# Kernel tuning notes

Measured on AMD Instinct MI355X. Metric: run time of the kernel, lower is better.

## Reference

```python
import jax, jax.numpy as jnp
import numpy as np

H = 512  # hidden_dim

def setup_inputs() -> dict:
    key = jax.random.key(0)
    k1, k2, k3, k4, k5 = jax.random.split(key, 5)
    B, S = 32, 2048
    hidden = jax.random.normal(k1, (B, 2 * H), dtype=jnp.float32)
    encoder_outputs = jax.random.normal(k2, (B, S, 2 * H), dtype=jnp.float32)
    # nn.Linear(4H, H): weight [H, 4H], bias [H]
    W = jax.random.normal(k3, (H, 4 * H), dtype=jnp.float32) / np.sqrt(4 * H)
    b = jnp.zeros((H,), dtype=jnp.float32)
    v = jax.random.normal(k4, (H,), dtype=jnp.float32) / np.sqrt(H)
    return {"hidden": hidden, "encoder_outputs": encoder_outputs, "W": W, "b": b, "v": v}

def reference(hidden, encoder_outputs, W, b, v):
    B, S, _ = encoder_outputs.shape
    # concat repeated decoder hidden with encoder outputs: [B, S, 4H]
    hidden_rep = jnp.broadcast_to(hidden[:, None, :], (B, S, hidden.shape[-1]))
    cat = jnp.concatenate([hidden_rep, encoder_outputs], axis=-1)
    energy = jnp.tanh(jnp.einsum('bsf,hf->bsh', cat, W) + b)  # [B, S, H]
    scores = jnp.einsum('bsh,h->bs', energy, v)               # [B, S]
    attn = jax.nn.softmax(scores, axis=1)                     # softmax over seq
    context = jnp.einsum('bsd,bs->bd', encoder_outputs, attn) # [B, 2H]
    return context
```

## Files before the change

### kernel.cpp

```cpp
#include <hip/hip_runtime.h>


typedef __fp16   half2v __attribute__((ext_vector_type(2)));
typedef _Float16 half8  __attribute__((ext_vector_type(8)));
typedef __attribute__((ext_vector_type(4)))  float f4;
typedef __attribute__((ext_vector_type(16))) float f16v;
typedef __attribute__((ext_vector_type(4)))  unsigned int uint4v;

__device__ __forceinline__ void gload_lds16(const void* g, void* l) {
    __builtin_amdgcn_global_load_lds(
        (const __attribute__((address_space(1))) unsigned int*)g,
        (__attribute__((address_space(3))) unsigned int*)l, 16, 0, 0);
}
__device__ __forceinline__ unsigned int bc2(half2v h) {
    return __builtin_bit_cast(unsigned int, h);
}

__global__ __launch_bounds__(256) void prep_kernel(
    const float* __restrict__ hidden, const float* __restrict__ W,
    const float* __restrict__ bias, float* __restrict__ u,
    unsigned short* __restrict__ w2) {
    if (blockIdx.x < 64) {
        int t = blockIdx.x * 256 + threadIdx.x;
        int b = t >> 9, h = t & 511;
        const f4* wr = (const f4*)(W + (size_t)h * 2048);
        const f4* hr = (const f4*)(hidden + (size_t)b * 1024);
        float acc = bias[h];
        #pragma unroll 4
        for (int i = 0; i < 256; ++i) {
            f4 w4 = wr[i]; f4 h4 = hr[i];
            acc += w4[0]*h4[0] + w4[1]*h4[1] + w4[2]*h4[2] + w4[3]*h4[3];
        }
        u[t] = acc;
    } else {
        int g = (blockIdx.x - 64) * 256 + threadIdx.x;
        int kk = g >> 11, id = g & 2047;
        int ntg = id >> 7, kh = (id >> 6) & 1, l = id & 63;
        int h = (ntg << 5) + (l & 31);
        int kg = 1024 + (kk << 5) + (kh << 4) + ((l >> 5) << 3);
        const float* src = W + (size_t)h * 2048 + kg;
        f4 x0 = *(const f4*)src;
        f4 x1 = *(const f4*)(src + 4);
        half8 vh;
        #pragma unroll
        for (int j = 0; j < 4; ++j) vh[j] = (_Float16)x0[j];
        #pragma unroll
        for (int j = 0; j < 4; ++j) vh[4 + j] = (_Float16)x1[j];
        ((half8*)w2)[g] = vh;
    }
}

__global__ __launch_bounds__(256, 3) void score_kernel(
    const float* __restrict__ enc, const unsigned short* __restrict__ w2,
    const float* __restrict__ u, const float* __restrict__ v,
    float* __restrict__ scores_part) {
    __shared__ short Ahi[2048], Alo[2048];
    __shared__ short Bs[8192];
    __shared__ float u_s[256], v_s[256];
    __shared__ float partial[4][64];

    const int tid  = threadIdx.x;
    const int wl   = tid >> 6, lane = tid & 63;
    const int col  = lane & 31;
    const int sblk = blockIdx.x >> 1, hh = blockIdx.x & 1;
    const int row0 = sblk * 64;
    const int b    = row0 >> 11;
    const float* encB = enc + (size_t)row0 * 1024;

    u_s[tid] = u[(b << 9) + (hh << 8) + tid];
    v_s[tid] = v[(hh << 8) + tid];

    f16v acc[2][2];
    #pragma unroll
    for (int mt = 0; mt < 2; ++mt)
        #pragma unroll
        for (int nt = 0; nt < 2; ++nt)
            #pragma unroll
            for (int r = 0; r < 16; ++r) acc[mt][nt][r] = 0.f;

    const int s_mt = tid >> 7, s_kh = (tid >> 6) & 1, s_l = tid & 63;
    const int s_row = (s_mt << 5) + (s_l & 31);
    const int s_kb  = (s_kh << 4) + ((s_l >> 5) << 3);
    const float* aSrc = encB + (size_t)s_row * 1024 + s_kb;

    const half8* Ah8 = (const half8*)Ahi;
    const half8* Al8 = (const half8*)Alo;
    const half8* Bh8 = (const half8*)Bs;

    for (int kk = 0; kk < 32; ++kk) {
        f4 x0 = *(const f4*)(aSrc + (kk << 5));
        f4 x1 = *(const f4*)(aSrc + (kk << 5) + 4);
        __syncthreads();
        {
            half2v h01 = __builtin_amdgcn_cvt_pkrtz(x0[0], x0[1]);
            half2v h23 = __builtin_amdgcn_cvt_pkrtz(x0[2], x0[3]);
            half2v h45 = __builtin_amdgcn_cvt_pkrtz(x1[0], x1[1]);
            half2v h67 = __builtin_amdgcn_cvt_pkrtz(x1[2], x1[3]);
            half2v l01 = __builtin_amdgcn_cvt_pkrtz(x0[0] - (float)h01[0], x0[1] - (float)h01[1]);
            half2v l23 = __builtin_amdgcn_cvt_pkrtz(x0[2] - (float)h23[0], x0[3] - (float)h23[1]);
            half2v l45 = __builtin_amdgcn_cvt_pkrtz(x1[0] - (float)h45[0], x1[1] - (float)h45[1]);
            half2v l67 = __builtin_amdgcn_cvt_pkrtz(x1[2] - (float)h67[0], x1[3] - (float)h67[1]);
            uint4v hp = {bc2(h01), bc2(h23), bc2(h45), bc2(h67)};
            uint4v lp = {bc2(l01), bc2(l23), bc2(l45), bc2(l67)};
            ((uint4v*)Ahi)[tid] = hp;
            ((uint4v*)Alo)[tid] = lp;
        }
        {
            const char* bsrc = (const char*)w2 + (size_t)kk * 32768 + (hh << 14)
                               + (wl << 12) + lane * 16;
            char* bdst = (char*)Bs + (wl << 12);
            #pragma unroll
            for (int i = 0; i < 4; ++i)
                gload_lds16(bsrc + (i << 10), bdst + (i << 10));
        }
        __syncthreads();
        #pragma unroll
        for (int kh = 0; kh < 2; ++kh) {
            half8 ah0 = Ah8[(kh << 6) + lane];
            half8 ah1 = Ah8[128 + (kh << 6) + lane];
            half8 al0 = Al8[(kh << 6) + lane];
            half8 al1 = Al8[128 + (kh << 6) + lane];
            #pragma unroll
            for (int nt = 0; nt < 2; ++nt) {
                int ntl = (wl << 1) + nt;
                half8 b8 = Bh8[((ntl << 1) + kh) * 64 + lane];
                acc[0][nt] = __builtin_amdgcn_mfma_f32_32x32x16_f16(ah0, b8, acc[0][nt], 0, 0, 0);
                acc[0][nt] = __builtin_amdgcn_mfma_f32_32x32x16_f16(al0, b8, acc[0][nt], 0, 0, 0);
                acc[1][nt] = __builtin_amdgcn_mfma_f32_32x32x16_f16(ah1, b8, acc[1][nt], 0, 0, 0);
                acc[1][nt] = __builtin_amdgcn_mfma_f32_32x32x16_f16(al1, b8, acc[1][nt], 0, 0, 0);
            }
        }
    }
    const int rhalf = (lane >> 5) << 2;
    #pragma unroll
    for (int mt = 0; mt < 2; ++mt) {
        #pragma unroll
        for (int reg = 0; reg < 16; ++reg) {
            float ssum = 0.f;
            #pragma unroll
            for (int nt = 0; nt < 2; ++nt) {
                int hl = (((wl << 1) + nt) << 5) + col;
                float x = u_s[hl] + acc[mt][nt][reg];
                float t = __expf(2.f * x);
                float th = 1.f - 2.f / (t + 1.f);
                ssum += v_s[hl] * th;
            }
            ssum += __shfl_xor(ssum, 1);
            ssum += __shfl_xor(ssum, 2);
            ssum += __shfl_xor(ssum, 4);
            ssum += __shfl_xor(ssum, 8);
            ssum += __shfl_xor(ssum, 16);
            if (col == 0)
                partial[wl][(mt << 5) + (reg & 3) + ((reg >> 2) << 3) + rhalf] = ssum;
        }
    }
    __syncthreads();
    if (tid < 64) {
        float s = partial[0][tid] + partial[1][tid] + partial[2][tid] + partial[3][tid];
        scores_part[(hh << 16) + row0 + tid] = s;
    }
}

__global__ __launch_bounds__(256) void ctx_partial_kernel(
    const float* __restrict__ enc, const float* __restrict__ scores_part,
    float* __restrict__ partials) {
    __shared__ float p_s[2048];
    __shared__ float wredm[4], wreds[4];
    const int t = threadIdx.x;
    const int b = blockIdx.x >> 5, sc = blockIdx.x & 31;
    const int wid = t >> 6, lane = t & 63;
    const float* s0 = scores_part + ((size_t)b << 11);
    const float* s1 = s0 + 65536;

    float vals[8];
    float mx = -1e30f;
    #pragma unroll
    for (int i = 0; i < 8; ++i) {
        int idx = t + (i << 8);
        vals[i] = s0[idx] + s1[idx];
        mx = fmaxf(mx, vals[i]);
    }
    #pragma unroll
    for (int off = 1; off < 64; off <<= 1) mx = fmaxf(mx, __shfl_xor(mx, off));
    if (lane == 0) wredm[wid] = mx;
    __syncthreads();
    mx = fmaxf(fmaxf(wredm[0], wredm[1]), fmaxf(wredm[2], wredm[3]));

    float lsum = 0.f;
    #pragma unroll
    for (int i = 0; i < 8; ++i) {
        float e = __expf(vals[i] - mx);
        p_s[t + (i << 8)] = e;
        lsum += e;
    }
    #pragma unroll
    for (int off = 1; off < 64; off <<= 1) lsum += __shfl_xor(lsum, off);
    if (lane == 0) wreds[wid] = lsum;
    __syncthreads();
    const float inv = 1.f / (wreds[0] + wreds[1] + wreds[2] + wreds[3]);

    f4 a = (f4){0.f, 0.f, 0.f, 0.f};
    const f4* erow = ((const f4*)(enc + ((size_t)b * 2048 + (sc << 6)) * 1024)) + t;
    #pragma unroll 4
    for (int i = 0; i < 64; ++i) {
        float p = p_s[(sc << 6) + i] * inv;
        f4 e = erow[(size_t)i << 8];
        a += p * e;
    }
    f4* dst = (f4*)(partials + (((size_t)(sc << 5) + b) << 10));
    dst[t] = a;
}

__global__ __launch_bounds__(256) void ctx_reduce_kernel(
    const float* __restrict__ partials, float* __restrict__ out) {
    int i = blockIdx.x * 256 + threadIdx.x;
    float s = 0.f;
    #pragma unroll
    for (int sc = 0; sc < 32; ++sc) s += partials[sc * 32768 + i];
    out[i] = s;
}

extern "C" void kernel_launch(void* const* d_in, const int* in_sizes, int n_in,
                              void* d_out, int out_size, void* d_ws, size_t ws_size,
                              hipStream_t stream) {
    const float* hidden = (const float*)d_in[0];
    const float* enc    = (const float*)d_in[1];
    const float* W      = (const float*)d_in[2];
    const float* bias   = (const float*)d_in[3];
    const float* v      = (const float*)d_in[4];
    float* out = (float*)d_out;
    char* ws = (char*)d_ws;

    float* u            = (float*)(ws);
    float* scores_part  = (float*)(ws + 65536);
    float* partials     = (float*)(ws + 589824);
    unsigned short* w2  = (unsigned short*)(ws + 4784128);

    prep_kernel<<<320, 256, 0, stream>>>(hidden, W, bias, u, w2);
    score_kernel<<<2048, 256, 0, stream>>>(enc, w2, u, v, scores_part);
    ctx_partial_kernel<<<1024, 256, 0, stream>>>(enc, scores_part, partials);
    ctx_reduce_kernel<<<128, 256, 0, stream>>>(partials, out);
}
```

Measured before the change: 548.0 us.

## Double-buffer score GEMM LDS, warp-parallel u projection, dual accumulators in context

The score kernel's K loop becomes software-pipelined. A and B tiles are double-buffered in LDS, the B tile for the next step is prefetched with global-to-LDS loads, and A registers are prefetched two steps ahead. Manual waitcnt plus a single barrier per step replaces the two __syncthreads, and MFMA priority is raised. The prep kernel's hidden·W projection now uses one wavefront per output row with coalesced loads and shuffle reduction instead of one thread per output. The context partial loop gets two accumulators, with the normalisation moved out of the loop. Doubled LDS use may lower occupancy of the 3-blocks-per-CU score kernel.

```diff
diff --git a/kernel.cpp b/kernel.cpp
--- a/kernel.cpp
+++ b/kernel.cpp
@@ -15,25 +15,15 @@
 __device__ __forceinline__ unsigned int bc2(half2v h) {
     return __builtin_bit_cast(unsigned int, h);
 }
+#define MEMPIN asm volatile("" ::: "memory")
 
 __global__ __launch_bounds__(256) void prep_kernel(
     const float* __restrict__ hidden, const float* __restrict__ W,
     const float* __restrict__ bias, float* __restrict__ u,
     unsigned short* __restrict__ w2) {
-    if (blockIdx.x < 64) {
-        int t = blockIdx.x * 256 + threadIdx.x;
-        int b = t >> 9, h = t & 511;
-        const f4* wr = (const f4*)(W + (size_t)h * 2048);
-        const f4* hr = (const f4*)(hidden + (size_t)b * 1024);
-        float acc = bias[h];
-        #pragma unroll 4
-        for (int i = 0; i < 256; ++i) {
-            f4 w4 = wr[i]; f4 h4 = hr[i];
-            acc += w4[0]*h4[0] + w4[1]*h4[1] + w4[2]*h4[2] + w4[3]*h4[3];
-        }
-        u[t] = acc;
-    } else {
-        int g = (blockIdx.x - 64) * 256 + threadIdx.x;
+    __shared__ float hid_s[1024];
+    if (blockIdx.x < 256) {
+        int g = blockIdx.x * 256 + threadIdx.x;
         int kk = g >> 11, id = g & 2047;
         int ntg = id >> 7, kh = (id >> 6) & 1, l = id & 63;
         int h = (ntg << 5) + (l & 31);
@@ -47,6 +37,29 @@
         #pragma unroll
         for (int j = 0; j < 4; ++j) vh[4 + j] = (_Float16)x1[j];
         ((half8*)w2)[g] = vh;
+    } else {
+        const int t = threadIdx.x;
+        const int blk = (int)blockIdx.x - 256;
+        const int b = blk >> 3, hg = blk & 7;
+        ((f4*)hid_s)[t] = ((const f4*)(hidden + ((size_t)b << 10)))[t];
+        __syncthreads();
+        const int w = t >> 6, lane = t & 63;
+        const f4* hid4 = (const f4*)hid_s;
+        #pragma unroll 2
+        for (int i = 0; i < 16; ++i) {
+            int h = (hg << 6) + (w << 4) + i;
+            const f4* wr = (const f4*)(W + (size_t)h * 2048);
+            float p = 0.f;
+            #pragma unroll
+            for (int i2 = 0; i2 < 4; ++i2) {
+                f4 w4 = wr[lane + (i2 << 6)];
+                f4 h4 = hid4[lane + (i2 << 6)];
+                p += w4[0]*h4[0] + w4[1]*h4[1] + w4[2]*h4[2] + w4[3]*h4[3];
+            }
+            #pragma unroll
+            for (int off = 1; off < 64; off <<= 1) p += __shfl_xor(p, off);
+            if (lane == 0) u[((size_t)b << 9) + h] = bias[h] + p;
+        }
     }
 }
 
@@ -54,8 +67,8 @@
     const float* __restrict__ enc, const unsigned short* __restrict__ w2,
     const float* __restrict__ u, const float* __restrict__ v,
     float* __restrict__ scores_part) {
-    __shared__ short Ahi[2048], Alo[2048];
-    __shared__ short Bs[8192];
+    __shared__ short Ahi[2][2048], Alo[2][2048];
+    __shared__ short Bs[2][8192];
     __shared__ float u_s[256], v_s[256];
     __shared__ float partial[4][64];
 
@@ -83,54 +96,99 @@
     const int s_kb  = (s_kh << 4) + ((s_l >> 5) << 3);
     const float* aSrc = encB + (size_t)s_row * 1024 + s_kb;
 
-    const half8* Ah8 = (const half8*)Ahi;
-    const half8* Al8 = (const half8*)Alo;
-    const half8* Bh8 = (const half8*)Bs;
-
-    for (int kk = 0; kk < 32; ++kk) {
-        f4 x0 = *(const f4*)(aSrc + (kk << 5));
-        f4 x1 = *(const f4*)(aSrc + (kk << 5) + 4);
-        __syncthreads();
-        {
-            half2v h01 = __builtin_amdgcn_cvt_pkrtz(x0[0], x0[1]);
-            half2v h23 = __builtin_amdgcn_cvt_pkrtz(x0[2], x0[3]);
-            half2v h45 = __builtin_amdgcn_cvt_pkrtz(x1[0], x1[1]);
-            half2v h67 = __builtin_amdgcn_cvt_pkrtz(x1[2], x1[3]);
-            half2v l01 = __builtin_amdgcn_cvt_pkrtz(x0[0] - (float)h01[0], x0[1] - (float)h01[1]);
-            half2v l23 = __builtin_amdgcn_cvt_pkrtz(x0[2] - (float)h23[0], x0[3] - (float)h23[1]);
-            half2v l45 = __builtin_amdgcn_cvt_pkrtz(x1[0] - (float)h45[0], x1[1] - (float)h45[1]);
-            half2v l67 = __builtin_amdgcn_cvt_pkrtz(x1[2] - (float)h67[0], x1[3] - (float)h67[1]);
-            uint4v hp = {bc2(h01), bc2(h23), bc2(h45), bc2(h67)};
-            uint4v lp = {bc2(l01), bc2(l23), bc2(l45), bc2(l67)};
-            ((uint4v*)Ahi)[tid] = hp;
-            ((uint4v*)Alo)[tid] = lp;
-        }
-        {
-            const char* bsrc = (const char*)w2 + (size_t)kk * 32768 + (hh << 14)
-                               + (wl << 12) + lane * 16;
-            char* bdst = (char*)Bs + (wl << 12);
-            #pragma unroll
-            for (int i = 0; i < 4; ++i)
-                gload_lds16(bsrc + (i << 10), bdst + (i << 10));
-        }
-        __syncthreads();
-        #pragma unroll
-        for (int kh = 0; kh < 2; ++kh) {
-            half8 ah0 = Ah8[(kh << 6) + lane];
-            half8 ah1 = Ah8[128 + (kh << 6) + lane];
-            half8 al0 = Al8[(kh << 6) + lane];
-            half8 al1 = Al8[128 + (kh << 6) + lane];
-            #pragma unroll
-            for (int nt = 0; nt < 2; ++nt) {
-                int ntl = (wl << 1) + nt;
-                half8 b8 = Bh8[((ntl << 1) + kh) * 64 + lane];
-                acc[0][nt] = __builtin_amdgcn_mfma_f32_32x32x16_f16(ah0, b8, acc[0][nt], 0, 0, 0);
-                acc[0][nt] = __builtin_amdgcn_mfma_f32_32x32x16_f16(al0, b8, acc[0][nt], 0, 0, 0);
-                acc[1][nt] = __builtin_amdgcn_mfma_f32_32x32x16_f16(ah1, b8, acc[1][nt], 0, 0, 0);
-                acc[1][nt] = __builtin_amdgcn_mfma_f32_32x32x16_f16(al1, b8, acc[1][nt], 0, 0, 0);
-            }
-        }
-    }
+#define STAGE_B(buf, kkex) do {                                               \
+        const char* bsrc_ = (const char*)w2 + (size_t)(kkex) * 32768          \
+                            + (hh << 14) + (wl << 12) + lane * 16;            \
+        char* bdst_ = (char*)(&Bs[buf][0]) + (wl << 12);                      \
+        gload_lds16(bsrc_,        bdst_);                                     \
+        gload_lds16(bsrc_ + 1024, bdst_ + 1024);                              \
+        gload_lds16(bsrc_ + 2048, bdst_ + 2048);                              \
+        gload_lds16(bsrc_ + 3072, bdst_ + 3072);                              \
+    } while (0)
+
+#define CVT_WRITE_A(buf, r0, r1) do {                                         \
+        half2v h01 = __builtin_amdgcn_cvt_pkrtz(r0[0], r0[1]);                \
+        half2v h23 = __builtin_amdgcn_cvt_pkrtz(r0[2], r0[3]);                \
+        half2v h45 = __builtin_amdgcn_cvt_pkrtz(r1[0], r1[1]);                \
+        half2v h67 = __builtin_amdgcn_cvt_pkrtz(r1[2], r1[3]);                \
+        half2v l01 = __builtin_amdgcn_cvt_pkrtz(r0[0] - (float)h01[0], r0[1] - (float)h01[1]); \
+        half2v l23 = __builtin_amdgcn_cvt_pkrtz(r0[2] - (float)h23[0], r0[3] - (float)h23[1]); \
+        half2v l45 = __builtin_amdgcn_cvt_pkrtz(r1[0] - (float)h45[0], r1[1] - (float)h45[1]); \
+        half2v l67 = __builtin_amdgcn_cvt_pkrtz(r1[2] - (float)h67[0], r1[3] - (float)h67[1]); \
+        uint4v hp_ = {bc2(h01), bc2(h23), bc2(h45), bc2(h67)};                \
+        uint4v lp_ = {bc2(l01), bc2(l23), bc2(l45), bc2(l67)};                \
+        ((uint4v*)(&Ahi[buf][0]))[tid] = hp_;                                 \
+        ((uint4v*)(&Alo[buf][0]))[tid] = lp_;                                 \
+    } while (0)
+
+#define COMPUTE(buf) do {                                                     \
+        const half8* Ah8_ = (const half8*)(&Ahi[buf][0]);                     \
+        const half8* Al8_ = (const half8*)(&Alo[buf][0]);                     \
+        const half8* Bh8_ = (const half8*)(&Bs[buf][0]);                      \
+        __builtin_amdgcn_s_setprio(1);                                        \
+        _Pragma("unroll")                                                     \
+        for (int kh = 0; kh < 2; ++kh) {                                      \
+            half8 ah0 = Ah8_[(kh << 6) + lane];                               \
+            half8 ah1 = Ah8_[128 + (kh << 6) + lane];                         \
+            half8 al0 = Al8_[(kh << 6) + lane];                               \
+            half8 al1 = Al8_[128 + (kh << 6) + lane];                         \
+            _Pragma("unroll")                                                 \
+            for (int nt = 0; nt < 2; ++nt) {                                  \
+                int ntl = (wl << 1) + nt;                                     \
+                half8 b8 = Bh8_[((ntl << 1) + kh) * 64 + lane];               \
+                acc[0][nt] = __builtin_amdgcn_mfma_f32_32x32x16_f16(ah0, b8, acc[0][nt], 0, 0, 0); \
+                acc[0][nt] = __builtin_amdgcn_mfma_f32_32x32x16_f16(al0, b8, acc[0][nt], 0, 0, 0); \
+                acc[1][nt] = __builtin_amdgcn_mfma_f32_32x32x16_f16(ah1, b8, acc[1][nt], 0, 0, 0); \
+                acc[1][nt] = __builtin_amdgcn_mfma_f32_32x32x16_f16(al1, b8, acc[1][nt], 0, 0, 0); \
+            }                                                                 \
+        }                                                                     \
+        __builtin_amdgcn_s_setprio(0);                                        \
+    } while (0)
+
+#define ITER(kkex, curlit, cx0, cx1, lx0, lx1) do {                           \
+        STAGE_B(curlit ^ 1, (kkex) + 1);                                      \
+        MEMPIN;                                                               \
+        int kc_ = (kkex) + 2; if (kc_ > 31) kc_ = 31;                         \
+        lx0 = *(const f4*)(aSrc + (kc_ << 5));                                \
+        lx1 = *(const f4*)(aSrc + (kc_ << 5) + 4);                            \
+        MEMPIN;                                                               \
+        COMPUTE(curlit);                                                      \
+        asm volatile("s_waitcnt vmcnt(6)" ::: "memory");                      \
+        CVT_WRITE_A(curlit ^ 1, cx0, cx1);                                    \
+        asm volatile("s_waitcnt vmcnt(2) lgkmcnt(0)" ::: "memory");           \
+        __builtin_amdgcn_s_barrier();                                         \
+        __builtin_amdgcn_sched_barrier(0);                                    \
+    } while (0)
+
+    f4 xa0, xa1, xb0, xb1;
+    {
+        f4 z0 = *(const f4*)(aSrc);
+        f4 z1 = *(const f4*)(aSrc + 4);
+        MEMPIN;
+        STAGE_B(0, 0);
+        MEMPIN;
+        xa0 = *(const f4*)(aSrc + 32);
+        xa1 = *(const f4*)(aSrc + 36);
+        MEMPIN;
+        CVT_WRITE_A(0, z0, z1);
+        asm volatile("s_waitcnt vmcnt(2) lgkmcnt(0)" ::: "memory");
+        __builtin_amdgcn_s_barrier();
+        __builtin_amdgcn_sched_barrier(0);
+    }
+
+    #pragma unroll 1
+    for (int kk = 0; kk < 30; kk += 2) {
+        ITER(kk,     0, xa0, xa1, xb0, xb1);
+        ITER(kk + 1, 1, xb0, xb1, xa0, xa1);
+    }
+    ITER(30, 0, xa0, xa1, xb0, xb1);
+    COMPUTE(1);
+
+#undef ITER
+#undef COMPUTE
+#undef CVT_WRITE_A
+#undef STAGE_B
+
     const int rhalf = (lane >> 5) << 2;
     #pragma unroll
     for (int mt = 0; mt < 2; ++mt) {
@@ -199,14 +257,15 @@
     __syncthreads();
     const float inv = 1.f / (wreds[0] + wreds[1] + wreds[2] + wreds[3]);
 
-    f4 a = (f4){0.f, 0.f, 0.f, 0.f};
+    f4 a0 = (f4){0.f, 0.f, 0.f, 0.f};
+    f4 a1 = (f4){0.f, 0.f, 0.f, 0.f};
     const f4* erow = ((const f4*)(enc + ((size_t)b * 2048 + (sc << 6)) * 1024)) + t;
-    #pragma unroll 4
-    for (int i = 0; i < 64; ++i) {
-        float p = p_s[(sc << 6) + i] * inv;
-        f4 e = erow[(size_t)i << 8];
-        a += p * e;
-    }
+    #pragma unroll 8
+    for (int i = 0; i < 64; i += 2) {
+        a0 += p_s[(sc << 6) + i]     * erow[(size_t)i << 8];
+        a1 += p_s[(sc << 6) + i + 1] * erow[((size_t)(i + 1)) << 8];
+    }
+    f4 a = (a0 + a1) * inv;
     f4* dst = (f4*)(partials + (((size_t)(sc << 5) + b) << 10));
     dst[t] = a;
 }
@@ -236,7 +295,7 @@
     float* partials     = (float*)(ws + 589824);
     unsigned short* w2  = (unsigned short*)(ws + 4784128);
 
-    prep_kernel<<<320, 256, 0, stream>>>(hidden, W, bias, u, w2);
+    prep_kernel<<<512, 256, 0, stream>>>(hidden, W, bias, u, w2);
     score_kernel<<<2048, 256, 0, stream>>>(enc, w2, u, v, scores_part);
     ctx_partial_kernel<<<1024, 256, 0, stream>>>(enc, scores_part, partials);
     ctx_reduce_kernel<<<128, 256, 0, stream>>>(partials, out);
```

Result: no change. 547.9 us (-0.0%).
